# Performance work log

Hardware: AMD Instinct MI355X
Metric: run time of the kernel (lower is better)

## Reference

```python
import jax, jax.numpy as jnp
import numpy as np
from jax import lax

C = 64
EPS = 1e-5


def _layernorm_c(x, g, b):
    # LayerNorm over channel dim of NCHW tensor (matches nn.LayerNorm([C]) applied on NHWC)
    mu = jnp.mean(x, axis=1, keepdims=True)
    var = jnp.var(x, axis=1, keepdims=True)
    xn = (x - mu) * lax.rsqrt(var + EPS)
    return xn * g[None, :, None, None] + b[None, :, None, None]


def _conv1x1(x, w, b):
    # w: [O, I]
    return jnp.einsum('bihw,oi->bohw', x, w) + b[None, :, None, None]


def _dwconv3x3(x, w, b):
    # depthwise 3x3, w: [C, 3, 3]
    k = w[:, None, :, :]  # OIHW with I=1
    y = lax.conv_general_dilated(x, k, (1, 1), 'SAME',
                                 feature_group_count=w.shape[0],
                                 dimension_numbers=('NCHW', 'OIHW', 'NCHW'))
    return y + b[None, :, None, None]


def setup_inputs() -> dict:
    key = jax.random.key(0)
    ks = jax.random.split(key, 24)
    s = 0.02
    d = {}
    d['x'] = jax.random.normal(ks[0], (4, C, 64, 64), dtype=jnp.float32)
    # CTA params
    d['cta_ln_g'] = jnp.ones((C,), jnp.float32)
    d['cta_ln_b'] = jnp.zeros((C,), jnp.float32)
    d['q_w'] = jax.random.normal(ks[1], (C, C), jnp.float32) * s
    d['q_b'] = jnp.zeros((C,), jnp.float32)
    d['k_w'] = jax.random.normal(ks[2], (C, 3, 3), jnp.float32) * s
    d['k_b'] = jnp.zeros((C,), jnp.float32)
    d['v_w'] = jax.random.normal(ks[3], (C, 3, 3), jnp.float32) * s
    d['v_b'] = jnp.zeros((C,), jnp.float32)
    d['cta_out_w'] = jax.random.normal(ks[4], (C, C), jnp.float32) * s
    d['cta_out_b'] = jnp.zeros((C,), jnp.float32)
    # NLE params
    d['nle_ln_g'] = jnp.ones((C,), jnp.float32)
    d['nle_ln_b'] = jnp.zeros((C,), jnp.float32)
    d['b1_w1'] = jax.random.normal(ks[5], (2 * C, C), jnp.float32) * s
    d['b1_b1'] = jnp.zeros((2 * C,), jnp.float32)
    d['b1_w2'] = jax.random.normal(ks[6], (2 * C, 3, 3), jnp.float32) * s
    d['b1_b2'] = jnp.zeros((2 * C,), jnp.float32)
    d['b2_w1'] = jax.random.normal(ks[7], (2 * C, C), jnp.float32) * s
    d['b2_b1'] = jnp.zeros((2 * C,), jnp.float32)
    d['b2_w2'] = jax.random.normal(ks[8], (2 * C, 3, 3), jnp.float32) * s
    d['b2_b2'] = jnp.zeros((2 * C,), jnp.float32)
    d['nle_out_w'] = jax.random.normal(ks[9], (C, 2 * C), jnp.float32) * s
    d['nle_out_b'] = jnp.zeros((C,), jnp.float32)
    return d


def csam_forward(x, cta_ln_g, cta_ln_b, q_w, q_b, k_w, k_b, v_w, v_b, cta_out_w, cta_out_b,
                 nle_ln_g, nle_ln_b, b1_w1, b1_b1, b1_w2, b1_b2, b2_w1, b2_b1, b2_w2, b2_b2,
                 nle_out_w, nle_out_b):
    B, Cc, H, W = x.shape
    scale = jnp.sqrt(jnp.float32(Cc))
    # --- CTA ---
    xn = _layernorm_c(x, cta_ln_g, cta_ln_b)
    q = _conv1x1(xn, q_w, q_b).reshape(B, Cc, H * W)      # [B,C,N]
    k = _dwconv3x3(xn, k_w, k_b).reshape(B, Cc, H * W)    # [B,C,N]
    v = _dwconv3x3(xn, v_w, v_b).reshape(B, Cc, H * W)    # [B,C,N]
    attn = jnp.einsum('bcn,bcm->bnm', q, k) / scale        # [B,N,N]
    attn = jax.nn.softmax(attn, axis=-1)
    out = jnp.einsum('bnm,bcm->bcn', attn, v).reshape(B, Cc, H, W)
    x_att = _conv1x1(out, cta_out_w, cta_out_b) + x
    # --- NLE ---
    xn2 = _layernorm_c(x_att, nle_ln_g, nle_ln_b)
    br1 = jax.nn.gelu(_dwconv3x3(_conv1x1(xn2, b1_w1, b1_b1), b1_w2, b1_b2), approximate=False)
    br2 = jax.nn.gelu(_dwconv3x3(_conv1x1(xn2, b2_w1, b2_b1), b2_w2, b2_b2), approximate=False)
    nle = _conv1x1(br1 * br2, nle_out_w, nle_out_b)
    return nle + x_att


def reference(x, cta_ln_g, cta_ln_b, q_w, q_b, k_w, k_b, v_w, v_b, cta_out_w, cta_out_b,
              nle_ln_g, nle_ln_b, b1_w1, b1_b1, b1_w2, b1_b2, b2_w1, b2_b1, b2_w2, b2_b2,
              nle_out_w, nle_out_b):
    return csam_forward(x, cta_ln_g, cta_ln_b, q_w, q_b, k_w, k_b, v_w, v_b, cta_out_w, cta_out_b,
                        nle_ln_g, nle_ln_b, b1_w1, b1_b1, b1_w2, b1_b2, b2_w1, b2_b1, b2_w2, b2_b2,
                        nle_out_w, nle_out_b)
```

## Files before the change

### kernel.cpp

```cpp
#include <hip/hip_runtime.h>
#include <hip/hip_bf16.h>
#include <math.h>

#define NPIX 4096
#define CH 64
#define BATCH 4
#define NSPLIT 4

typedef __attribute__((ext_vector_type(8))) short short8;
typedef __attribute__((ext_vector_type(4))) float f32x4;
typedef __attribute__((ext_vector_type(4))) unsigned short us4;
typedef __attribute__((ext_vector_type(4))) unsigned int u32x4;

static __device__ __forceinline__ unsigned short f2bf(float f) {
  union { float f; unsigned u; } v; v.f = f;
  unsigned u = v.u;
  unsigned r = u + 0x7FFF + ((u >> 16) & 1);
  return (unsigned short)(r >> 16);
}
static __device__ __forceinline__ float bf2f(unsigned short u) {
  union { unsigned u; float f; } v; v.u = ((unsigned)u) << 16; return v.f;
}
static __device__ __forceinline__ unsigned cvtpk(float lo, float hi) {
  unsigned r;
  asm("v_cvt_pk_bf16_f32 %0, %1, %2" : "=v"(r) : "v"(lo), "v"(hi));
  return r;
}

__global__ __launch_bounds__(256) void k_ln_q(
    const float* __restrict__ x, const float* __restrict__ lg, const float* __restrict__ lb,
    const float* __restrict__ qw, const float* __restrict__ qb,
    float* __restrict__ xn, unsigned short* __restrict__ Q)
{
  __shared__ float xT[64][64];
  __shared__ unsigned short xB[64][64];
  int tid = threadIdx.x, px = tid & 63, g4 = tid >> 6;
  int idx0 = blockIdx.x * 64;
  int idx = idx0 + px;
  int b = idx >> 12, p = idx & 4095;
  const float* xb = x + (size_t)b * CH * NPIX + p;
  for (int j = 0; j < 16; ++j) { int c = 16 * g4 + j; xT[c][px] = xb[(size_t)c * NPIX]; }
  __syncthreads();
  float xv[64]; float s = 0.f;
#pragma unroll
  for (int c = 0; c < 64; ++c) { xv[c] = xT[c][px]; s += xv[c]; }
  float mu = s * (1.f / 64.f), vs = 0.f;
#pragma unroll
  for (int c = 0; c < 64; ++c) { float d = xv[c] - mu; vs += d * d; }
  float rs = rsqrtf(vs * (1.f / 64.f) + 1e-5f);
#pragma unroll
  for (int c = 0; c < 64; ++c) xv[c] = (xv[c] - mu) * rs * lg[c] + lb[c];

  float* xnb = xn + (size_t)b * CH * NPIX + p;
#define LNQ_WR(C0)                                                             \
  {                                                                            \
    unsigned short t[16];                                                      \
    _Pragma("unroll") for (int j = 0; j < 16; ++j) {                           \
      float v = xv[C0 + j];                                                    \
      xnb[(size_t)(C0 + j) * NPIX] = v;                                        \
      t[j] = f2bf(v);                                                          \
    }                                                                          \
    *(short8*)&xB[px][(((C0 / 8) + 0) ^ (px & 7)) * 8] = *(short8*)t;          \
    *(short8*)&xB[px][(((C0 / 8) + 1) ^ (px & 7)) * 8] = *(short8*)(t + 8);    \
  }
  if (g4 == 0) LNQ_WR(0)
  else if (g4 == 1) LNQ_WR(16)
  else if (g4 == 2) LNQ_WR(32)
  else LNQ_WR(48)
#undef LNQ_WR
  __syncthreads();

  int lane = tid & 63, l15 = lane & 15, gg = lane >> 4;
  short8 af[2];
#pragma unroll
  for (int kc = 0; kc < 2; ++kc) {
    const float* wp = qw + (size_t)(g4 * 16 + l15) * 64 + kc * 32 + 8 * gg;
    unsigned short t[8];
#pragma unroll
    for (int j = 0; j < 8; ++j) t[j] = f2bf(wp[j]);
    af[kc] = *(short8*)t;
  }
  float bv[4];
#pragma unroll
  for (int r = 0; r < 4; ++r) bv[r] = qb[g4 * 16 + 4 * gg + r];
#pragma unroll
  for (int ct = 0; ct < 4; ++ct) {
    f32x4 acc = {bv[0], bv[1], bv[2], bv[3]};
    int row = ct * 16 + l15;
    short8 bf0 = *(const short8*)&xB[row][((0 + gg) ^ (row & 7)) * 8];
    short8 bf1 = *(const short8*)&xB[row][((4 + gg) ^ (row & 7)) * 8];
    acc = __builtin_amdgcn_mfma_f32_16x16x32_bf16(af[0], bf0, acc, 0, 0, 0);
    acc = __builtin_amdgcn_mfma_f32_16x16x32_bf16(af[1], bf1, acc, 0, 0, 0);
    us4 v;
#pragma unroll
    for (int r = 0; r < 4; ++r) v[r] = f2bf(acc[r] * 0.125f);
    *(us4*)(Q + (size_t)(idx0 + row) * 64 + g4 * 16 + 4 * gg) = v;
  }
}

__global__ __launch_bounds__(256) void k_dwkv(
    const float* __restrict__ xn,
    const float* __restrict__ kw, const float* __restrict__ kb,
    const float* __restrict__ vw, const float* __restrict__ vb,
    unsigned short* __restrict__ K, unsigned short* __restrict__ VT)
{
  int idx = blockIdx.x * 256 + threadIdx.x;
  int b = idx >> 12, p = idx & 4095;
  int h = p >> 6, w = p & 63;
  int c0 = blockIdx.y * 8;
  size_t base = (size_t)b * CH * NPIX;
  unsigned short kq[8];
#pragma unroll
  for (int j = 0; j < 8; ++j) {
    int c = c0 + j;
    const float* xc = xn + base + (size_t)c * NPIX;
    float ka = kb[c], va = vb[c];
#pragma unroll
    for (int dy = -1; dy <= 1; ++dy) {
#pragma unroll
      for (int dx = -1; dx <= 1; ++dx) {
        int hh = h + dy, ww = w + dx;
        float xvv = (hh >= 0 && hh < 64 && ww >= 0 && ww < 64) ? xc[hh * 64 + ww] : 0.f;
        int t = (dy + 1) * 3 + (dx + 1);
        ka += kw[c * 9 + t] * xvv;
        va += vw[c * 9 + t] * xvv;
      }
    }
    kq[j] = f2bf(ka);
    VT[((size_t)b * CH + c) * NPIX + p] = f2bf(va);
  }
  *(short8*)(K + (size_t)idx * 64 + c0) = *(short8*)(kq);
}

#define SW(r) ((((r) & 7) ^ (((r) >> 3) << 1)) & 7)
__global__ __launch_bounds__(256, 4) void k_attn(
    const unsigned short* __restrict__ Q, const unsigned short* __restrict__ K,
    const unsigned short* __restrict__ VT, unsigned short* __restrict__ OPb,
    float* __restrict__ LS)
{
  __shared__ unsigned short kls[2][64][64];
  __shared__ unsigned short vls[2][64][64];

  int tid = threadIdx.x;
  int wid = tid >> 6, lane = tid & 63;
  int l15 = lane & 15, g = lane >> 4;
  int b = blockIdx.y, split = blockIdx.z;
  int nbase = blockIdx.x * 128 + wid * 32;

  const unsigned short* Qb = Q + (size_t)b * NPIX * CH;
  const unsigned short* Kb = K + (size_t)b * NPIX * CH;
  const unsigned short* Vb = VT + (size_t)b * CH * NPIX;

  short8 qf0a = *(const short8*)(Qb + (size_t)(nbase + l15) * CH + 8 * g);
  short8 qf1a = *(const short8*)(Qb + (size_t)(nbase + l15) * CH + 32 + 8 * g);
  short8 qf0b = *(const short8*)(Qb + (size_t)(nbase + 16 + l15) * CH + 8 * g);
  short8 qf1b = *(const short8*)(Qb + (size_t)(nbase + 16 + l15) * CH + 32 + 8 * g);

  f32x4 acca[4], accb[4];
#pragma unroll
  for (int i = 0; i < 4; ++i) {
    acca[i] = (f32x4){0.f, 0.f, 0.f, 0.f};
    accb[i] = (f32x4){0.f, 0.f, 0.f, 0.f};
  }
  float lsa = 0.f, lsb = 0.f;

  int srow = tid >> 3, sch = tid & 7;
  int srow1 = srow + 32;
  int wa0 = srow * 64 + ((sch ^ SW(srow)) * 8);
  int wa1 = srow1 * 64 + ((sch ^ SW(srow1)) * 8);
  const unsigned short* ksrc0 = Kb + (size_t)(split * 1024 + srow) * CH + sch * 8;
  const unsigned short* ksrc1 = Kb + (size_t)(split * 1024 + srow1) * CH + sch * 8;
  const unsigned short* vsrc0 = Vb + (size_t)srow * NPIX + split * 1024 + sch * 8;
  const unsigned short* vsrc1 = Vb + (size_t)srow1 * NPIX + split * 1024 + sch * 8;

  int kperm = 8 * (l15 >> 2) + (l15 & 3);

  short8 kg0, kg1, vg0, vg1;
  kg0 = *(const short8*)(ksrc0);
  kg1 = *(const short8*)(ksrc1);
  vg0 = *(const short8*)(vsrc0);
  vg1 = *(const short8*)(vsrc1);
  *(short8*)(&kls[0][0][0] + wa0) = kg0;
  *(short8*)(&kls[0][0][0] + wa1) = kg1;
  *(short8*)(&vls[0][0][0] + wa0) = vg0;
  *(short8*)(&vls[0][0][0] + wa1) = vg1;
  __syncthreads();

  for (int t = 0; t < 16; ++t) {
    if (t < 15) {
      int ko = (t + 1) * 64;
      kg0 = *(const short8*)(ksrc0 + (size_t)ko * CH);
      kg1 = *(const short8*)(ksrc1 + (size_t)ko * CH);
      vg0 = *(const short8*)(vsrc0 + ko);
      vg1 = *(const short8*)(vsrc1 + ko);
    }

    const unsigned short* kb = &kls[t & 1][0][0];
    const unsigned short* vb = &vls[t & 1][0][0];

#pragma unroll
    for (int s = 0; s < 2; ++s) {
      int r0 = s * 32 + kperm;
      int r1 = s * 32 + 4 + kperm;
      short8 kf00 = *(const short8*)(kb + r0 * 64 + (((0 + g) ^ SW(r0)) * 8));
      short8 kf01 = *(const short8*)(kb + r0 * 64 + (((4 + g) ^ SW(r0)) * 8));
      short8 kf10 = *(const short8*)(kb + r1 * 64 + (((0 + g) ^ SW(r1)) * 8));
      short8 kf11 = *(const short8*)(kb + r1 * 64 + (((4 + g) ^ SW(r1)) * 8));
      f32x4 sa0 = {0.f,0.f,0.f,0.f}, sa1 = {0.f,0.f,0.f,0.f};
      f32x4 sb0 = {0.f,0.f,0.f,0.f}, sb1 = {0.f,0.f,0.f,0.f};
      sa0 = __builtin_amdgcn_mfma_f32_16x16x32_bf16(kf00, qf0a, sa0, 0, 0, 0);
      sa0 = __builtin_amdgcn_mfma_f32_16x16x32_bf16(kf01, qf1a, sa0, 0, 0, 0);
      sa1 = __builtin_amdgcn_mfma_f32_16x16x32_bf16(kf10, qf0a, sa1, 0, 0, 0);
      sa1 = __builtin_amdgcn_mfma_f32_16x16x32_bf16(kf11, qf1a, sa1, 0, 0, 0);
      sb0 = __builtin_amdgcn_mfma_f32_16x16x32_bf16(kf00, qf0b, sb0, 0, 0, 0);
      sb0 = __builtin_amdgcn_mfma_f32_16x16x32_bf16(kf01, qf1b, sb0, 0, 0, 0);
      sb1 = __builtin_amdgcn_mfma_f32_16x16x32_bf16(kf10, qf0b, sb1, 0, 0, 0);
      sb1 = __builtin_amdgcn_mfma_f32_16x16x32_bf16(kf11, qf1b, sb1, 0, 0, 0);

      float a0 = __expf(sa0[0]), a1 = __expf(sa0[1]), a2 = __expf(sa0[2]), a3 = __expf(sa0[3]);
      float a4 = __expf(sa1[0]), a5 = __expf(sa1[1]), a6 = __expf(sa1[2]), a7 = __expf(sa1[3]);
      lsa += (a0 + a1) + (a2 + a3) + (a4 + a5) + (a6 + a7);
      u32x4 pka;
      pka[0] = cvtpk(a0, a1); pka[1] = cvtpk(a2, a3);
      pka[2] = cvtpk(a4, a5); pka[3] = cvtpk(a6, a7);
      short8 pa = *(short8*)&pka;

      float b0 = __expf(sb0[0]), b1 = __expf(sb0[1]), b2 = __expf(sb0[2]), b3 = __expf(sb0[3]);
      float b4 = __expf(sb1[0]), b5 = __expf(sb1[1]), b6 = __expf(sb1[2]), b7 = __expf(sb1[3]);
      lsb += (b0 + b1) + (b2 + b3) + (b4 + b5) + (b6 + b7);
      u32x4 pkb;
      pkb[0] = cvtpk(b0, b1); pkb[1] = cvtpk(b2, b3);
      pkb[2] = cvtpk(b4, b5); pkb[3] = cvtpk(b6, b7);
      short8 pbv = *(short8*)&pkb;

#pragma unroll
      for (int cs = 0; cs < 4; ++cs) {
        int row = cs * 16 + l15;
        short8 vf = *(const short8*)(vb + row * 64 + (((4 * s + g) ^ SW(row)) * 8));
        acca[cs] = __builtin_amdgcn_mfma_f32_16x16x32_bf16(vf, pa, acca[cs], 0, 0, 0);
        accb[cs] = __builtin_amdgcn_mfma_f32_16x16x32_bf16(vf, pbv, accb[cs], 0, 0, 0);
      }
    }

    if (t < 15) {
      unsigned short* kw_ = &kls[(t + 1) & 1][0][0];
      unsigned short* vw_ = &vls[(t + 1) & 1][0][0];
      *(short8*)(kw_ + wa0) = kg0;
      *(short8*)(kw_ + wa1) = kg1;
      *(short8*)(vw_ + wa0) = vg0;
      *(short8*)(vw_ + wa1) = vg1;
    }
    __syncthreads();
  }

  lsa += __shfl_xor(lsa, 16, 64);
  lsa += __shfl_xor(lsa, 32, 64);
  lsb += __shfl_xor(lsb, 16, 64);
  lsb += __shfl_xor(lsb, 32, 64);

  size_t sb_ = ((size_t)split * BATCH + b) * NPIX;
  unsigned short* Oba = OPb + (sb_ + nbase + l15) * 64;
  unsigned short* Obb = OPb + (sb_ + nbase + 16 + l15) * 64;
#pragma unroll
  for (int cs = 0; cs < 4; ++cs) {
    us4 va, vbq;
#pragma unroll
    for (int r = 0; r < 4; ++r) { va[r] = f2bf(acca[cs][r]); vbq[r] = f2bf(accb[cs][r]); }
    *(us4*)(Oba + cs * 16 + 4 * g) = va;
    *(us4*)(Obb + cs * 16 + 4 * g) = vbq;
  }
  if (g == 0) {
    LS[sb_ + nbase + l15] = lsa;
    LS[sb_ + nbase + 16 + l15] = lsb;
  }
}
#undef SW

__global__ __launch_bounds__(256) void k_proj_ln2_pw(
    const unsigned short* __restrict__ OPb, const float* __restrict__ LSv,
    const float* __restrict__ x,
    const float* __restrict__ ow, const float* __restrict__ ob,
    const float* __restrict__ lg, const float* __restrict__ lb,
    const float* __restrict__ w1, const float* __restrict__ bb1,
    const float* __restrict__ w2, const float* __restrict__ bb2,
    float* __restrict__ xatt, float* __restrict__ t1, float* __restrict__ t2)
{
  __shared__ unsigned short aT[64][64];
  __shared__ float sm1[4][4][16], sm2[4][4][16];
  int tid = threadIdx.x;
  int b = blockIdx.y, pxb = blockIdx.x * 64;

#pragma unroll
  for (int h = 0; h < 2; ++h) {
    int off = (h * 256 + tid) * 8;
    int px = off >> 6;
    float sv[8] = {0.f, 0.f, 0.f, 0.f, 0.f, 0.f, 0.f, 0.f};
    float ls = 0.f;
#pragma unroll
    for (int sp = 0; sp < NSPLIT; ++sp) {
      size_t sbase = ((size_t)(sp * BATCH + b) * NPIX + pxb);
      short8 a = *(const short8*)(OPb + sbase * 64 + off);
#pragma unroll
      for (int j = 0; j < 8; ++j) sv[j] += bf2f((unsigned short)a[j]);
      ls += LSv[sbase + px];
    }
    float inv = 1.f / ls;
    unsigned short t[8];
#pragma unroll
    for (int j = 0; j < 8; ++j) t[j] = f2bf(sv[j] * inv);
    *(short8*)&aT[px][(((tid & 7) ^ (px & 7)) * 8)] = *(short8*)t;
  }
  __syncthreads();

  int wid = tid >> 6, lane = tid & 63;
  int l15 = lane & 15, g = lane >> 4;

  short8 af[2];
#pragma unroll
  for (int kc = 0; kc < 2; ++kc) {
    const float* wp = ow + (size_t)(wid * 16 + l15) * 64 + kc * 32 + 8 * g;
    unsigned short t[8];
#pragma unroll
    for (int j = 0; j < 8; ++j) t[j] = f2bf(wp[j]);
    af[kc] = *(short8*)t;
  }
  float bv[4], lgv[4], lbv[4];
#pragma unroll
  for (int r = 0; r < 4; ++r) {
    int o = wid * 16 + 4 * g + r;
    bv[r] = ob[o]; lgv[r] = lg[o]; lbv[r] = lb[o];
  }
  f32x4 acc[4];
#pragma unroll
  for (int ct = 0; ct < 4; ++ct) acc[ct] = (f32x4){bv[0], bv[1], bv[2], bv[3]};
#pragma unroll
  for (int ct = 0; ct < 4; ++ct) {
    int row = ct * 16 + l15;
    short8 bf0 = *(const short8*)&aT[row][(((0 + g) ^ (row & 7)) * 8)];
    short8 bf1 = *(const short8*)&aT[row][(((4 + g) ^ (row & 7)) * 8)];
    acc[ct] = __builtin_amdgcn_mfma_f32_16x16x32_bf16(af[0], bf0, acc[ct], 0, 0, 0);
    acc[ct] = __builtin_amdgcn_mfma_f32_16x16x32_bf16(af[1], bf1, acc[ct], 0, 0, 0);
  }

  float xo[4][4];
#pragma unroll
  for (int ct = 0; ct < 4; ++ct) {
    int p = pxb + ct * 16 + l15;
    float s1 = 0.f, s2 = 0.f;
#pragma unroll
    for (int r = 0; r < 4; ++r) {
      int o = wid * 16 + 4 * g + r;
      size_t oi = ((size_t)b * CH + o) * NPIX + p;
      float v = acc[ct][r] + x[oi];
      xatt[oi] = v;
      xo[ct][r] = v;
      s1 += v; s2 += v * v;
    }
    s1 += __shfl_xor(s1, 16, 64); s1 += __shfl_xor(s1, 32, 64);
    s2 += __shfl_xor(s2, 16, 64); s2 += __shfl_xor(s2, 32, 64);
    if (g == 0) { sm1[wid][ct][l15] = s1; sm2[wid][ct][l15] = s2; }
  }
  __syncthreads();
  {
    int ckid = (wid * 16 + 4 * g) >> 3;
    int coff = (4 * g) & 7;
#pragma unroll
    for (int ct = 0; ct < 4; ++ct) {
      int row = ct * 16 + l15;
      float mu = (sm1[0][ct][l15] + sm1[1][ct][l15] + sm1[2][ct][l15] + sm1[3][ct][l15]) * (1.f / 64.f);
      float ms = (sm2[0][ct][l15] + sm2[1][ct][l15] + sm2[2][ct][l15] + sm2[3][ct][l15]) * (1.f / 64.f);
      float rs = rsqrtf(ms - mu * mu + 1e-5f);
      us4 v4;
#pragma unroll
      for (int r = 0; r < 4; ++r) v4[r] = f2bf((xo[ct][r] - mu) * rs * lgv[r] + lbv[r]);
      *(us4*)&aT[row][((ckid ^ (row & 7)) * 8) + coff] = v4;
    }
  }

  const float* W2  = (wid & 2) ? w2 : w1;
  const float* bb2_ = (wid & 2) ? bb2 : bb1;
  float* tdst      = (wid & 2) ? t2 : t1;
  int oh = (wid & 1) * 64;
  short8 af2[4][2];
#pragma unroll
  for (int ot = 0; ot < 4; ++ot)
#pragma unroll
    for (int kc = 0; kc < 2; ++kc) {
      const float* wp = W2 + (size_t)(oh + ot * 16 + l15) * 64 + kc * 32 + 8 * g;
      unsigned short tt[8];
#pragma unroll
      for (int j = 0; j < 8; ++j) tt[j] = f2bf(wp[j]);
      af2[ot][kc] = *(short8*)tt;
    }
  __syncthreads();

  f32x4 acc2[4][4];
#pragma unroll
  for (int ot = 0; ot < 4; ++ot) {
    float b0 = bb2_[oh + ot * 16 + 4 * g + 0];
    float b1 = bb2_[oh + ot * 16 + 4 * g + 1];
    float b2 = bb2_[oh + ot * 16 + 4 * g + 2];
    float b3 = bb2_[oh + ot * 16 + 4 * g + 3];
#pragma unroll
    for (int ct = 0; ct < 4; ++ct) acc2[ot][ct] = (f32x4){b0, b1, b2, b3};
  }
#pragma unroll
  for (int ct = 0; ct < 4; ++ct) {
    int row = ct * 16 + l15;
    short8 bf0 = *(const short8*)&aT[row][(((0 + g) ^ (row & 7)) * 8)];
    short8 bf1 = *(const short8*)&aT[row][(((4 + g) ^ (row & 7)) * 8)];
#pragma unroll
    for (int ot = 0; ot < 4; ++ot) {
      acc2[ot][ct] = __builtin_amdgcn_mfma_f32_16x16x32_bf16(af2[ot][0], bf0, acc2[ot][ct], 0, 0, 0);
      acc2[ot][ct] = __builtin_amdgcn_mfma_f32_16x16x32_bf16(af2[ot][1], bf1, acc2[ot][ct], 0, 0, 0);
    }
  }
#pragma unroll
  for (int ot = 0; ot < 4; ++ot)
#pragma unroll
    for (int ct = 0; ct < 4; ++ct) {
      int p = pxb + ct * 16 + l15;
#pragma unroll
      for (int r = 0; r < 4; ++r) {
        int o = oh + ot * 16 + 4 * g + r;
        tdst[((size_t)b * 128 + o) * NPIX + p] = acc2[ot][ct][r];
      }
    }
}

__global__ __launch_bounds__(256) void k_dwgelu(
    const float* __restrict__ t1, const float* __restrict__ t2,
    const float* __restrict__ w1, const float* __restrict__ bb1,
    const float* __restrict__ w2, const float* __restrict__ bb2,
    unsigned short* __restrict__ g12T)
{
  int idx = blockIdx.x * 256 + threadIdx.x;
  int b = idx >> 12, p = idx & 4095;
  int h = p >> 6, w = p & 63;
  int c0 = blockIdx.y * 8;
  unsigned short outv[8];
#pragma unroll
  for (int j = 0; j < 8; ++j) {
    int c = c0 + j;
    size_t tb = ((size_t)b * 128 + c) * NPIX;
    float a1 = bb1[c], a2 = bb2[c];
#pragma unroll
    for (int dy = -1; dy <= 1; ++dy) {
#pragma unroll
      for (int dx = -1; dx <= 1; ++dx) {
        int hh = h + dy, ww = w + dx;
        bool ok = (hh >= 0 && hh < 64 && ww >= 0 && ww < 64);
        float v1 = ok ? t1[tb + hh * 64 + ww] : 0.f;
        float v2 = ok ? t2[tb + hh * 64 + ww] : 0.f;
        int t = (dy + 1) * 3 + (dx + 1);
        a1 += w1[c * 9 + t] * v1;
        a2 += w2[c * 9 + t] * v2;
      }
    }
    float ge1 = 0.5f * a1 * (1.f + erff(a1 * 0.70710678118654752f));
    float ge2 = 0.5f * a2 * (1.f + erff(a2 * 0.70710678118654752f));
    outv[j] = f2bf(ge1 * ge2);
  }
  *(short8*)(g12T + (size_t)idx * 128 + c0) = *(short8*)outv;
}

__global__ __launch_bounds__(256) void k_out(
    const float* __restrict__ W, const float* __restrict__ bias,
    const unsigned short* __restrict__ InT, const float* __restrict__ res,
    float* __restrict__ outF)
{
  int tid = threadIdx.x;
  int wid = tid >> 6, lane = tid & 63;
  int l15 = lane & 15, g = lane >> 4;
  int b = blockIdx.y, pxb = blockIdx.x * 64;
  const unsigned short* In = InT + ((size_t)b * NPIX + pxb) * 128;

  short8 af[4];
#pragma unroll
  for (int kc = 0; kc < 4; ++kc) {
    const float* wp = W + (size_t)(wid * 16 + l15) * 128 + kc * 32 + 8 * g;
    unsigned short t[8];
#pragma unroll
    for (int j = 0; j < 8; ++j) t[j] = f2bf(wp[j]);
    af[kc] = *(short8*)t;
  }
  float bv[4];
#pragma unroll
  for (int r = 0; r < 4; ++r) bv[r] = bias[wid * 16 + 4 * g + r];
#pragma unroll
  for (int ct = 0; ct < 4; ++ct) {
    f32x4 acc = {bv[0], bv[1], bv[2], bv[3]};
#pragma unroll
    for (int kc = 0; kc < 4; ++kc) {
      short8 bf = *(const short8*)(In + (size_t)(ct * 16 + l15) * 128 + kc * 32 + 8 * g);
      acc = __builtin_amdgcn_mfma_f32_16x16x32_bf16(af[kc], bf, acc, 0, 0, 0);
    }
    int p = pxb + ct * 16 + l15;
#pragma unroll
    for (int r = 0; r < 4; ++r) {
      int o = wid * 16 + 4 * g + r;
      size_t oi = ((size_t)b * CH + o) * NPIX + p;
      outF[oi] = acc[r] + res[oi];
    }
  }
}

extern "C" void kernel_launch(void* const* d_in, const int* in_sizes, int n_in,
                              void* d_out, int out_size, void* d_ws, size_t ws_size,
                              hipStream_t stream) {
  const float* x        = (const float*)d_in[0];
  const float* cta_ln_g = (const float*)d_in[1];
  const float* cta_ln_b = (const float*)d_in[2];
  const float* q_w      = (const float*)d_in[3];
  const float* q_b      = (const float*)d_in[4];
  const float* k_w      = (const float*)d_in[5];
  const float* k_b      = (const float*)d_in[6];
  const float* v_w      = (const float*)d_in[7];
  const float* v_b      = (const float*)d_in[8];
  const float* cta_out_w= (const float*)d_in[9];
  const float* cta_out_b= (const float*)d_in[10];
  const float* nle_ln_g = (const float*)d_in[11];
  const float* nle_ln_b = (const float*)d_in[12];
  const float* b1_w1    = (const float*)d_in[13];
  const float* b1_b1    = (const float*)d_in[14];
  const float* b1_w2    = (const float*)d_in[15];
  const float* b1_b2    = (const float*)d_in[16];
  const float* b2_w1    = (const float*)d_in[17];
  const float* b2_b1    = (const float*)d_in[18];
  const float* b2_w2    = (const float*)d_in[19];
  const float* b2_b2    = (const float*)d_in[20];
  const float* nle_out_w= (const float*)d_in[21];
  const float* nle_out_b= (const float*)d_in[22];

  char* ws = (char*)d_ws;
  float*          xn   = (float*)(ws);
  unsigned short* Qb   = (unsigned short*)(ws + (4u  << 20));
  unsigned short* Kb   = (unsigned short*)(ws + (6u  << 20));
  unsigned short* VTb  = (unsigned short*)(ws + (8u  << 20));
  unsigned short* OPb  = (unsigned short*)(ws + (10u << 20));
  float*          LSb  = (float*)(ws + (18u << 20));
  float*          xatt = (float*)(ws + (21u << 20));
  float*          t1   = (float*)(ws + (27u << 20));
  float*          t2   = (float*)(ws + (35u << 20));
  unsigned short* g12T = (unsigned short*)(ws);

  k_ln_q        <<<256, 256, 0, stream>>>(x, cta_ln_g, cta_ln_b, q_w, q_b, xn, Qb);
  k_dwkv        <<<dim3(64, 8), 256, 0, stream>>>(xn, k_w, k_b, v_w, v_b, Kb, VTb);
  k_attn        <<<dim3(32, BATCH, NSPLIT), 256, 0, stream>>>(Qb, Kb, VTb, OPb, LSb);
  k_proj_ln2_pw <<<dim3(64, 4), 256, 0, stream>>>(OPb, LSb, x, cta_out_w, cta_out_b,
                                                  nle_ln_g, nle_ln_b,
                                                  b1_w1, b1_b1, b2_w1, b2_b1,
                                                  xatt, t1, t2);
  k_dwgelu      <<<dim3(64, 16), 256, 0, stream>>>(t1, t2, b1_w2, b1_b2, b2_w2, b2_b2, g12T);
  k_out         <<<dim3(64, 4), 256, 0, stream>>>(nle_out_w, nle_out_b, g12T, xatt, (float*)d_out);
}
```

Baseline: 70.57 us.

## Fuse depthwise conv+GELU gating into output projection via shared-memory tile

Merges the depthwise 3x3 conv, GELU gating and the final 1x1 output projection into one kernel. Each block computes one image row's gated activations into a swizzled LDS tile, then runs the MFMA projection directly from shared memory. This removes the bf16 intermediate round trip through global memory and one kernel launch. In exchange the grid shrinks from 1024 blocks to 256, and each thread now computes 32 channels serially, so the stencil and erf work has less parallelism.

Measured after the change: 83.43 us. +18.2%, slower.

```diff
diff --git a/kernel.cpp b/kernel.cpp
--- a/kernel.cpp
+++ b/kernel.cpp
@@ -428,53 +428,22 @@
     }
 }
 
-__global__ __launch_bounds__(256) void k_dwgelu(
+__global__ __launch_bounds__(256) void k_dwgelu_out(
     const float* __restrict__ t1, const float* __restrict__ t2,
     const float* __restrict__ w1, const float* __restrict__ bb1,
     const float* __restrict__ w2, const float* __restrict__ bb2,
-    unsigned short* __restrict__ g12T)
+    const float* __restrict__ W, const float* __restrict__ bias,
+    const float* __restrict__ res, float* __restrict__ outF)
 {
-  int idx = blockIdx.x * 256 + threadIdx.x;
-  int b = idx >> 12, p = idx & 4095;
-  int h = p >> 6, w = p & 63;
-  int c0 = blockIdx.y * 8;
-  unsigned short outv[8];
-#pragma unroll
-  for (int j = 0; j < 8; ++j) {
-    int c = c0 + j;
-    size_t tb = ((size_t)b * 128 + c) * NPIX;
-    float a1 = bb1[c], a2 = bb2[c];
-#pragma unroll
-    for (int dy = -1; dy <= 1; ++dy) {
-#pragma unroll
-      for (int dx = -1; dx <= 1; ++dx) {
-        int hh = h + dy, ww = w + dx;
-        bool ok = (hh >= 0 && hh < 64 && ww >= 0 && ww < 64);
-        float v1 = ok ? t1[tb + hh * 64 + ww] : 0.f;
-        float v2 = ok ? t2[tb + hh * 64 + ww] : 0.f;
-        int t = (dy + 1) * 3 + (dx + 1);
-        a1 += w1[c * 9 + t] * v1;
-        a2 += w2[c * 9 + t] * v2;
-      }
-    }
-    float ge1 = 0.5f * a1 * (1.f + erff(a1 * 0.70710678118654752f));
-    float ge2 = 0.5f * a2 * (1.f + erff(a2 * 0.70710678118654752f));
-    outv[j] = f2bf(ge1 * ge2);
-  }
-  *(short8*)(g12T + (size_t)idx * 128 + c0) = *(short8*)outv;
-}
-
-__global__ __launch_bounds__(256) void k_out(
-    const float* __restrict__ W, const float* __restrict__ bias,
-    const unsigned short* __restrict__ InT, const float* __restrict__ res,
-    float* __restrict__ outF)
-{
+  __shared__ unsigned short gT[64][128];
   int tid = threadIdx.x;
+  int b = blockIdx.y;
+  int hrow = blockIdx.x;
+  int pxb = hrow * 64;
+  int px = tid & 63, cg = tid >> 6;
+
   int wid = tid >> 6, lane = tid & 63;
   int l15 = lane & 15, g = lane >> 4;
-  int b = blockIdx.y, pxb = blockIdx.x * 64;
-  const unsigned short* In = InT + ((size_t)b * NPIX + pxb) * 128;
-
   short8 af[4];
 #pragma unroll
   for (int kc = 0; kc < 4; ++kc) {
@@ -487,15 +456,58 @@
   float bv[4];
 #pragma unroll
   for (int r = 0; r < 4; ++r) bv[r] = bias[wid * 16 + 4 * g + r];
+
+  {
+    int w = px;
+    bool okm = hrow > 0, okp = hrow < 63;
+    bool okl = w > 0, okr = w < 63;
+#pragma unroll
+    for (int jc = 0; jc < 32; jc += 4) {
+      us4 outv;
+#pragma unroll
+      for (int q = 0; q < 4; ++q) {
+        int c = cg * 32 + jc + q;
+        const float* s1 = t1 + ((size_t)b * 128 + c) * NPIX + hrow * 64 + w;
+        const float* s2 = t2 + ((size_t)b * 128 + c) * NPIX + hrow * 64 + w;
+        const float* w1c = w1 + c * 9;
+        const float* w2c = w2 + c * 9;
+        float a1 = bb1[c], a2 = bb2[c];
+#pragma unroll
+        for (int dy = -1; dy <= 1; ++dy) {
+          bool oky = (dy == 0) || (dy < 0 ? okm : okp);
+          int ro = dy * 64;
+#pragma unroll
+          for (int dx = -1; dx <= 1; ++dx) {
+            bool ok = oky && ((dx == 0) || (dx < 0 ? okl : okr));
+            float v1 = ok ? s1[ro + dx] : 0.f;
+            float v2 = ok ? s2[ro + dx] : 0.f;
+            int t = (dy + 1) * 3 + (dx + 1);
+            a1 += w1c[t] * v1;
+            a2 += w2c[t] * v2;
+          }
+        }
+        float ge1 = 0.5f * a1 * (1.f + erff(a1 * 0.70710678118654752f));
+        float ge2 = 0.5f * a2 * (1.f + erff(a2 * 0.70710678118654752f));
+        outv[q] = f2bf(ge1 * ge2);
+      }
+      int ch0 = cg * 32 + jc;
+      int ck = ch0 >> 3, coff = ch0 & 7;
+      *(us4*)&gT[px][((ck ^ (px & 7)) * 8) + coff] = outv;
+    }
+  }
+  __syncthreads();
+
 #pragma unroll
   for (int ct = 0; ct < 4; ++ct) {
     f32x4 acc = {bv[0], bv[1], bv[2], bv[3]};
+    int row = ct * 16 + l15;
 #pragma unroll
     for (int kc = 0; kc < 4; ++kc) {
-      short8 bf = *(const short8*)(In + (size_t)(ct * 16 + l15) * 128 + kc * 32 + 8 * g);
+      int ckr = kc * 4 + g;
+      short8 bf = *(const short8*)&gT[row][((ckr ^ (row & 7)) * 8)];
       acc = __builtin_amdgcn_mfma_f32_16x16x32_bf16(af[kc], bf, acc, 0, 0, 0);
     }
-    int p = pxb + ct * 16 + l15;
+    int p = pxb + row;
 #pragma unroll
     for (int r = 0; r < 4; ++r) {
       int o = wid * 16 + 4 * g + r;
@@ -542,7 +554,6 @@
   float*          xatt = (float*)(ws + (21u << 20));
   float*          t1   = (float*)(ws + (27u << 20));
   float*          t2   = (float*)(ws + (35u << 20));
-  unsigned short* g12T = (unsigned short*)(ws);
 
   k_ln_q        <<<256, 256, 0, stream>>>(x, cta_ln_g, cta_ln_b, q_w, q_b, xn, Qb);
   k_dwkv        <<<dim3(64, 8), 256, 0, stream>>>(xn, k_w, k_b, v_w, v_b, Kb, VTb);
@@ -551,6 +562,6 @@
                                                   nle_ln_g, nle_ln_b,
                                                   b1_w1, b1_b1, b2_w1, b2_b1,
                                                   xatt, t1, t2);
-  k_dwgelu      <<<dim3(64, 16), 256, 0, stream>>>(t1, t2, b1_w2, b1_b2, b2_w2, b2_b2, g12T);
-  k_out         <<<dim3(64, 4), 256, 0, stream>>>(nle_out_w, nle_out_b, g12T, xatt, (float*)d_out);
-}
+  k_dwgelu_out  <<<dim3(64, 4), 256, 0, stream>>>(t1, t2, b1_w2, b1_b2, b2_w2, b2_b2,
+                                                  nle_out_w, nle_out_b, xatt, (float*)d_out);
+}
```
